# Optimization experiments

Measured on AMD Instinct MI355X. Metric: run time of the kernel, lower is better.

## Reference

```python
import jax, jax.numpy as jnp
import numpy as np

B, T, V, H = 1024, 256, 256, 32
SIGMA = 0.01


def setup_inputs() -> dict:
    key = jax.random.key(0)
    k0, k1, k2, k3 = jax.random.split(key, 4)
    X = jax.random.randint(k0, (B, T), 0, V)  # token ids [batch, num_steps]
    W_xh = jax.random.normal(k1, (V, H), dtype=jnp.float32) * SIGMA
    W_hh = jax.random.normal(k2, (H, H), dtype=jnp.float32) * SIGMA
    b_h = jnp.zeros((H,), dtype=jnp.float32)
    W_hq = jax.random.normal(k3, (H, V), dtype=jnp.float32) * SIGMA
    b_q = jnp.zeros((V,), dtype=jnp.float32)
    return {"X": X, "W_xh": W_xh, "W_hh": W_hh, "b_h": b_h, "W_hq": W_hq, "b_q": b_q}


def reference(X, W_xh, W_hh, b_h, W_hq, b_q):
    # one_hot(X.T, V) @ W_xh  ==  row-gather of W_xh  -> [T, B, H] (time-major)
    x_emb = W_xh[X.T]
    h0 = jnp.zeros((X.shape[0], W_hh.shape[0]), dtype=W_hh.dtype)  # [B, H]

    def step(h, xe):
        h = jnp.tanh(xe + h @ W_hh + b_h)
        return h, h

    _, hs = jax.lax.scan(step, h0, x_emb)  # hs: [T, B, H]
    # output layer, stacked on axis 1 as in the torch code -> [B, T, V]
    logits = jnp.einsum('tbh,hv->btv', hs, W_hq) + b_q
    return logits
```

## Files before the change

kernel.cpp:

```cpp
#include <hip/hip_runtime.h>


#define B_SZ 1024
#define T_SZ 256
#define V_SZ 256
#define H_SZ 32
#define HIST_P 40

typedef _Float16 f16x8 __attribute__((ext_vector_type(8)));
typedef float    f32x4 __attribute__((ext_vector_type(4)));

__device__ __forceinline__ float lane_bcast(float v, int lane) {
    return __int_as_float(__builtin_amdgcn_readlane(__float_as_int(v), lane));
}

__device__ __forceinline__ float fast_tanh(float x) {
    float z = __expf(2.0f * x);
    return (z - 1.0f) * __builtin_amdgcn_rcpf(z + 1.0f);
}

__global__ __launch_bounds__(256, 1) void rnnlm_fused(
    const int*   __restrict__ X,
    const float* __restrict__ W_xh,
    const float* __restrict__ W_hh,
    const float* __restrict__ b_h,
    const float* __restrict__ W_hq,
    const float* __restrict__ b_q,
    float*       __restrict__ out)
{
    __shared__ __align__(16) _Float16 s_whqT[V_SZ][H_SZ];
    __shared__ __align__(16) _Float16 s_hist[4][T_SZ][HIST_P];

    const int tid   = threadIdx.x;
    const int wv    = tid >> 6;
    const int lane  = tid & 63;
    const int l15   = lane & 15;
    const int kg    = lane >> 4;
    const int batch = blockIdx.x * 4 + wv;

    #pragma unroll
    for (int k = 0; k < H_SZ; ++k)
        s_whqT[tid][k] = (_Float16)W_hq[k * V_SZ + tid];
    __syncthreads();

    f16x8 bfrag[16];
    float bq16[16];
    #pragma unroll
    for (int vt = 0; vt < 16; ++vt) {
        bfrag[vt] = *(const f16x8*)&s_whqT[vt * 16 + l15][kg * 8];
        bq16[vt]  = b_q[vt * 16 + l15];
    }

    if (lane < H_SZ) {
        float whh[H_SZ];
        #pragma unroll
        for (int i = 0; i < H_SZ; ++i)
            whh[i] = W_hh[i * H_SZ + lane];
        const float bh = b_h[lane];

        const int* Xr = X + batch * T_SZ;
        int   tkA = Xr[3], tkB = Xr[4], tkC = Xr[5];
        float e0 = W_xh[Xr[0] * H_SZ + lane];
        float e1 = W_xh[Xr[1] * H_SZ + lane];
        float e2 = W_xh[Xr[2] * H_SZ + lane];

        float h = 0.0f;
        for (int t = 0; t < T_SZ; ++t) {
            float a0 = e0 + bh, a1 = 0.0f, a2 = 0.0f, a3 = 0.0f;
            e0 = e1; e1 = e2;
            e2 = W_xh[tkA * H_SZ + lane];
            tkA = tkB; tkB = tkC;
            tkC = Xr[t + 6 < T_SZ ? t + 6 : T_SZ - 1];

            #pragma unroll
            for (int i = 0; i < H_SZ; i += 4) {
                a0 += lane_bcast(h, i + 0) * whh[i + 0];
                a1 += lane_bcast(h, i + 1) * whh[i + 1];
                a2 += lane_bcast(h, i + 2) * whh[i + 2];
                a3 += lane_bcast(h, i + 3) * whh[i + 3];
            }
            h = fast_tanh((a0 + a1) + (a2 + a3));
            s_hist[wv][t][lane] = (_Float16)h;
        }
    }

    #pragma unroll
    for (int ti = 0; ti < 16; ++ti) {
        const int t0 = ti * 16;
        const f16x8 afrag = *(const f16x8*)&s_hist[wv][t0 + l15][kg * 8];
        float* p = out + ((size_t)batch * T_SZ + t0 + 4 * kg) * V_SZ + l15;
        #pragma unroll
        for (int vt = 0; vt < 16; ++vt) {
            f32x4 acc = { bq16[vt], bq16[vt], bq16[vt], bq16[vt] };
            acc = __builtin_amdgcn_mfma_f32_16x16x32_f16(afrag, bfrag[vt], acc,
                                                         0, 0, 0);
            p[0 * V_SZ + vt * 16] = acc[0];
            p[1 * V_SZ + vt * 16] = acc[1];
            p[2 * V_SZ + vt * 16] = acc[2];
            p[3 * V_SZ + vt * 16] = acc[3];
        }
    }
}

extern "C" void kernel_launch(void* const* d_in, const int* in_sizes, int n_in,
                              void* d_out, int out_size, void* d_ws, size_t ws_size,
                              hipStream_t stream) {
    const int*   X    = (const int*)d_in[0];
    const float* W_xh = (const float*)d_in[1];
    const float* W_hh = (const float*)d_in[2];
    const float* b_h  = (const float*)d_in[3];
    const float* W_hq = (const float*)d_in[4];
    const float* b_q  = (const float*)d_in[5];
    float* out = (float*)d_out;

    rnnlm_fused<<<dim3(B_SZ / 4), dim3(256), 0, stream>>>(X, W_xh, W_hh, b_h,
                                                          W_hq, b_q, out);
}
```

Measured before the change: 313.7 us.

## Interleave recurrence chunks with output MFMA and write logits as float4

The recurrence now runs in 16-step chunks, and each chunk's hidden states are projected to logits right away through a double-buffered shared-memory history. Before, all 256 steps finished before any output was written. Swapping the MFMA operands makes each lane hold four consecutive vocab columns, so the stores become 16-byte vector writes instead of scalar ones. The aim is to overlap the global store traffic with the serial recurrence and to issue fewer, wider stores. The trade-off is per-chunk control flow, and the lanes that skip the recurrence sit idle while the others compute.

New measurement: 304.9 us. 2.8% less time.

```diff
diff --git a/kernel.cpp b/kernel.cpp
--- a/kernel.cpp
+++ b/kernel.cpp
@@ -5,7 +5,9 @@
 #define T_SZ 256
 #define V_SZ 256
 #define H_SZ 32
-#define HIST_P 40
+#define HP   40
+#define NCH  16
+#define CS   16
 
 typedef _Float16 f16x8 __attribute__((ext_vector_type(8)));
 typedef float    f32x4 __attribute__((ext_vector_type(4)));
@@ -29,7 +31,7 @@
     float*       __restrict__ out)
 {
     __shared__ __align__(16) _Float16 s_whqT[V_SZ][H_SZ];
-    __shared__ __align__(16) _Float16 s_hist[4][T_SZ][HIST_P];
+    __shared__ __align__(16) _Float16 s_hist[4][2][CS][HP];
 
     const int tid   = threadIdx.x;
     const int wv    = tid >> 6;
@@ -43,61 +45,66 @@
         s_whqT[tid][k] = (_Float16)W_hq[k * V_SZ + tid];
     __syncthreads();
 
-    f16x8 bfrag[16];
-    float bq16[16];
+    f16x8 aw[16];
+    f32x4 bq4[16];
     #pragma unroll
     for (int vt = 0; vt < 16; ++vt) {
-        bfrag[vt] = *(const f16x8*)&s_whqT[vt * 16 + l15][kg * 8];
-        bq16[vt]  = b_q[vt * 16 + l15];
+        aw[vt]  = *(const f16x8*)&s_whqT[vt * 16 + l15][kg * 8];
+        bq4[vt] = *(const f32x4*)(b_q + vt * 16 + 4 * kg);
     }
 
+    float whh[H_SZ];
+    float bh = 0.0f, h = 0.0f;
+    float e0 = 0.0f, e1 = 0.0f, e2 = 0.0f;
+    int   tkA = 0, tkB = 0, tkC = 0;
+    const int* Xr = X + batch * T_SZ;
     if (lane < H_SZ) {
-        float whh[H_SZ];
         #pragma unroll
         for (int i = 0; i < H_SZ; ++i)
             whh[i] = W_hh[i * H_SZ + lane];
-        const float bh = b_h[lane];
-
-        const int* Xr = X + batch * T_SZ;
-        int   tkA = Xr[3], tkB = Xr[4], tkC = Xr[5];
-        float e0 = W_xh[Xr[0] * H_SZ + lane];
-        float e1 = W_xh[Xr[1] * H_SZ + lane];
-        float e2 = W_xh[Xr[2] * H_SZ + lane];
-
-        float h = 0.0f;
-        for (int t = 0; t < T_SZ; ++t) {
-            float a0 = e0 + bh, a1 = 0.0f, a2 = 0.0f, a3 = 0.0f;
-            e0 = e1; e1 = e2;
-            e2 = W_xh[tkA * H_SZ + lane];
-            tkA = tkB; tkB = tkC;
-            tkC = Xr[t + 6 < T_SZ ? t + 6 : T_SZ - 1];
-
-            #pragma unroll
-            for (int i = 0; i < H_SZ; i += 4) {
-                a0 += lane_bcast(h, i + 0) * whh[i + 0];
-                a1 += lane_bcast(h, i + 1) * whh[i + 1];
-                a2 += lane_bcast(h, i + 2) * whh[i + 2];
-                a3 += lane_bcast(h, i + 3) * whh[i + 3];
-            }
-            h = fast_tanh((a0 + a1) + (a2 + a3));
-            s_hist[wv][t][lane] = (_Float16)h;
-        }
+        bh  = b_h[lane];
+        tkA = Xr[3]; tkB = Xr[4]; tkC = Xr[5];
+        e0 = W_xh[Xr[0] * H_SZ + lane];
+        e1 = W_xh[Xr[1] * H_SZ + lane];
+        e2 = W_xh[Xr[2] * H_SZ + lane];
     }
 
-    #pragma unroll
-    for (int ti = 0; ti < 16; ++ti) {
-        const int t0 = ti * 16;
-        const f16x8 afrag = *(const f16x8*)&s_hist[wv][t0 + l15][kg * 8];
-        float* p = out + ((size_t)batch * T_SZ + t0 + 4 * kg) * V_SZ + l15;
+    float* outb = out + (size_t)batch * T_SZ * V_SZ;
+
+    for (int c = 0; c < NCH; ++c) {
+        const int buf = c & 1;
+
+        if (lane < H_SZ) {
+            for (int s = 0; s < CS; ++s) {
+                const int t = c * CS + s;
+                float a0 = e0 + bh, a1 = 0.0f, a2 = 0.0f, a3 = 0.0f;
+                e0 = e1; e1 = e2;
+                e2 = W_xh[tkA * H_SZ + lane];
+                tkA = tkB; tkB = tkC;
+                tkC = Xr[t + 6 < T_SZ ? t + 6 : T_SZ - 1];
+
+                #pragma unroll
+                for (int i = 0; i < H_SZ; i += 4) {
+                    a0 += lane_bcast(h, i + 0) * whh[i + 0];
+                    a1 += lane_bcast(h, i + 1) * whh[i + 1];
+                    a2 += lane_bcast(h, i + 2) * whh[i + 2];
+                    a3 += lane_bcast(h, i + 3) * whh[i + 3];
+                }
+                h = fast_tanh((a0 + a1) + (a2 + a3));
+                s_hist[wv][buf][s][lane] = (_Float16)h;
+            }
+        }
+        asm volatile("" ::: "memory");
+
+        const f16x8 hfrag = *(const f16x8*)&s_hist[wv][buf][l15][kg * 8];
+
+        float* p = outb + ((size_t)(c * CS + l15)) * V_SZ + 4 * kg;
         #pragma unroll
         for (int vt = 0; vt < 16; ++vt) {
-            f32x4 acc = { bq16[vt], bq16[vt], bq16[vt], bq16[vt] };
-            acc = __builtin_amdgcn_mfma_f32_16x16x32_f16(afrag, bfrag[vt], acc,
+            f32x4 acc = bq4[vt];
+            acc = __builtin_amdgcn_mfma_f32_16x16x32_f16(aw[vt], hfrag, acc,
                                                          0, 0, 0);
-            p[0 * V_SZ + vt * 16] = acc[0];
-            p[1 * V_SZ + vt * 16] = acc[1];
-            p[2 * V_SZ + vt * 16] = acc[2];
-            p[3 * V_SZ + vt * 16] = acc[3];
+            *(f32x4*)(p + vt * 16) = acc;
         }
     }
 }
```
